# Optimization experiments

Hardware: AMD Instinct MI355X
Metric: run time of the kernel (lower is better)

Reference implementation:

```python
import jax, jax.numpy as jnp
import numpy as np

S_STRIDE = 4
NS = 4
SHIFT_RANGE = 2 * NS + 1  # 9 -> 81 shifts
MASK_THRESH = 10.0


def setup_inputs() -> dict:
    key = jax.random.key(0)
    k1, k2, k3, k4 = jax.random.split(key, 4)
    N, C, H, W = 2, 8, 1024, 1024
    ms_img = jax.random.uniform(k1, (N, C, H, W), dtype=jnp.float32)
    target = jax.random.uniform(k2, (N, C, H, W), dtype=jnp.float32)
    ms_img_o = jax.random.uniform(k3, (N, C, H, W), dtype=jnp.float32)
    fr_pan = jax.random.uniform(k4, (N, 1, H, W), dtype=jnp.float32)
    return {"ms_img": ms_img, "target": target, "ms_img_o": ms_img_o, "fr_pan": fr_pan}


def _min_shift_loss(ms_img, target):
    # Equivalent to torch: reflect-pad target, unfold 9x9 dilated-by-4 windows,
    # per-shift sum_C |ms - shifted_target|, then min over the 81 shifts.
    # Computed with a running min to avoid the (N,C,81,H,W) intermediate.
    N, C, H, W = target.shape
    p = NS * S_STRIDE
    tpad = jnp.pad(target, ((0, 0), (0, 0), (p, p), (p, p)), mode="reflect")
    min_sloss = None
    for i in range(SHIFT_RANGE):
        for j in range(SHIFT_RANGE):
            shifted = tpad[:, :, i * S_STRIDE:i * S_STRIDE + H, j * S_STRIDE:j * S_STRIDE + W]
            sl = jnp.sum(jnp.abs(ms_img - shifted), axis=1)  # (N, H, W)
            min_sloss = sl if min_sloss is None else jnp.minimum(min_sloss, sl)
    return min_sloss


def _normalize(x):
    # min-max normalize to [0,1] over the whole tensor (normalize_torch)
    lo = jnp.min(x)
    hi = jnp.max(x)
    return (x - lo) / (hi - lo)


def reference(ms_img, target, ms_img_o, fr_pan):
    min_sloss = _min_shift_loss(ms_img, target)           # (N, H, W)
    ms_o_gray = jnp.mean(ms_img_o, axis=1)                # (N, H, W)
    mask_gray = _normalize(jnp.abs(ms_o_gray - fr_pan[:, 0])) * 255.0
    mask = mask_gray > MASK_THRESH
    masked_sum = jnp.sum(jnp.where(mask, min_sloss, 0.0))
    cnt = jnp.sum(mask).astype(min_sloss.dtype)
    # mean over masked pixels; 0 if mask empty (matches torch early-return 0)
    return jnp.where(cnt > 0, masked_sum / jnp.maximum(cnt, 1.0), 0.0)
```

## Files before the change

### kernel.cpp

```cpp
#include <hip/hip_runtime.h>

#define WW 1024
#define HH 1024
#define NIMG 2
#define NCH 8
#define HWSZ (HH * WW)
#define CHW (NCH * HWSZ)
#define NBLK_MASK 2048
#define NBLK_MAIN 1024
#define WS_SUM 4096
#define WS_CNT 4097
#define WS_TKT 4098
#define WS_DV16 4352
#define WS_QT (4352 + HWSZ)
#define RECU4 320
#define SLOTU 1280

typedef unsigned int uint;

__device__ __forceinline__ uint pknorm(float a, float b) {
    uint d;
    asm("v_cvt_pknorm_u16_f32 %0, %1, %2" : "=v"(d) : "v"(a), "v"(b));
    return d;
}
__device__ __forceinline__ uint sadu8(uint a, uint b, uint c) {
    uint d;
    asm("v_sad_u8 %0, %1, %2, %3" : "=v"(d) : "v"(a), "v"(b), "v"(c));
    return d;
}
__device__ __forceinline__ uint q8(float x) {
    return (uint)__float2int_rn(x * 255.f);
}
__device__ __forceinline__ int reflect_idx(int t) {
    if (t < 0) t = -t;
    if (t > HH - 1) t = 2 * (HH - 1) - t;
    return t;
}
__device__ __forceinline__ int gp2slot(int gp) {
    return (gp & 1) ? (68 + (gp >> 1)) : (gp >> 1);
}

#define GLD16(g, l)                                                         \
    __builtin_amdgcn_global_load_lds(                                       \
        (const __attribute__((address_space(1))) uint*)(g),                 \
        (__attribute__((address_space(3))) uint*)(l), 16, 0, 0)

__global__ __launch_bounds__(256) void k_quant(const float* __restrict__ tgt,
                                               uint4* __restrict__ qt4) {
    int b = blockIdx.x;
    int t = threadIdx.x;
    int row = b & 1023;
    int np = b >> 10;
    int n = np >> 1, p = np & 1;
    const float* c0 = tgt + (size_t)(n * NCH + 4 * p) * HWSZ + (size_t)row * WW;

    float4 v0 = *(const float4*)(c0 + 4 * t);
    float4 v1 = *(const float4*)(c0 + HWSZ + 4 * t);
    float4 v2 = *(const float4*)(c0 + 2 * HWSZ + 4 * t);
    float4 v3 = *(const float4*)(c0 + 3 * HWSZ + 4 * t);
    uint4 u;
    u.x = q8(v0.x) | (q8(v1.x) << 8) | (q8(v2.x) << 16) | (q8(v3.x) << 24);
    u.y = q8(v0.y) | (q8(v1.y) << 8) | (q8(v2.y) << 16) | (q8(v3.y) << 24);
    u.z = q8(v0.z) | (q8(v1.z) << 8) | (q8(v2.z) << 16) | (q8(v3.z) << 24);
    u.w = q8(v0.w) | (q8(v1.w) << 8) | (q8(v2.w) << 16) | (q8(v3.w) << 24);

    size_t rb = ((size_t)((n << 10) + row)) * 2;
    int h1 = t >> 7;
    int gp = (t & 127) + 4;
    qt4[(rb + h1) * RECU4 + p * 136 + gp2slot(gp)] = u;
    if (t >= 124 && t < 128)
        qt4[(rb + 1) * RECU4 + p * 136 + gp2slot(t - 124)] = u;
    if (t >= 128 && t < 132)
        qt4[(rb + 0) * RECU4 + p * 136 + gp2slot(t - 128 + 132)] = u;
    if (t < 32) {
        int which = t >> 4, m = t & 15;
        int pc = which ? (528 + m) : m;
        int j = which ? (1022 - m) : (16 - m);
        uint val = q8(c0[j]) | (q8(c0[j + HWSZ]) << 8) |
                   (q8(c0[j + 2 * HWSZ]) << 16) | (q8(c0[j + 3 * HWSZ]) << 24);
        uint* recU = (uint*)(qt4 + (rb + which) * RECU4);
        recU[p * 544 + gp2slot(pc >> 2) * 4 + (pc & 3)] = val;
    }
}

__global__ __launch_bounds__(256) void k_mask(const float* __restrict__ msO,
                                              const float* __restrict__ pan,
                                              float* __restrict__ wsF,
                                              uint* __restrict__ dv16) {
    int b = blockIdx.x;
    int gid = b * 256 + threadIdx.x;
    int base = gid * 4;
    int n = base >> 20;
    int hw = base & (HWSZ - 1);
    const float* po = msO + (size_t)n * CHW + hw;
    float sx = 0.f, sy = 0.f, sz = 0.f, sw = 0.f;
#pragma unroll
    for (int c = 0; c < NCH; ++c) {
        float4 v = *(const float4*)(po + c * HWSZ);
        sx += v.x; sy += v.y; sz += v.z; sw += v.w;
    }
    float4 pv = *(const float4*)(pan + (size_t)n * HWSZ + hw);
    float4 d;
    d.x = fabsf(sx * 0.125f - pv.x);
    d.y = fabsf(sy * 0.125f - pv.y);
    d.z = fabsf(sz * 0.125f - pv.z);
    d.w = fabsf(sw * 0.125f - pv.w);
    uint2 dpk;
    dpk.x = pknorm(d.x, d.y);
    dpk.y = pknorm(d.z, d.w);
    *(uint2*)(dv16 + (base >> 1)) = dpk;

    float m = fminf(fminf(d.x, d.y), fminf(d.z, d.w));
    float M = fmaxf(fmaxf(d.x, d.y), fmaxf(d.z, d.w));
#pragma unroll
    for (int off = 32; off > 0; off >>= 1) {
        m = fminf(m, __shfl_down(m, off));
        M = fmaxf(M, __shfl_down(M, off));
    }
    __shared__ float sm[4], sM[4];
    int wid = threadIdx.x >> 6, lane = threadIdx.x & 63;
    if (lane == 0) { sm[wid] = m; sM[wid] = M; }
    __syncthreads();
    if (threadIdx.x == 0) {
        wsF[b] = fminf(fminf(sm[0], sm[1]), fminf(sm[2], sm[3]));
        wsF[2048 + b] = fmaxf(fmaxf(sM[0], sM[1]), fmaxf(sM[2], sM[3]));
        if (b == 0) {
            wsF[WS_SUM] = 0.f;
            wsF[WS_CNT] = 0.f;
            ((unsigned*)wsF)[WS_TKT] = 0u;
        }
    }
}

__global__ __launch_bounds__(64) void k_main(const float* __restrict__ ms,
                                             const uint4* __restrict__ qt4,
                                             float* __restrict__ wsF,
                                             const uint* __restrict__ dv16,
                                             float* __restrict__ out) {
    __shared__ __align__(16) uint ldsU[10 * SLOTU];
    const int t = threadIdx.x;
    const int b = blockIdx.x;
    const int xcd = b & 7;
    const int q = b >> 3;
    const int n = q >> 6;
    const int r = q & 63;
    const int hb = r >> 5;
    const int w = r & 31;
    const int h0 = xcd * 128 + 16 * (w >> 2) + (w & 3);
    const int w0 = hb * 512 + 8 * t;

    float lmin = 1.0e38f, lmax = -1.0e38f;
#pragma unroll
    for (int k = 0; k < 8; ++k) {
        float4 v = ((const float4*)wsF)[k * 64 + t];
        float4 x = ((const float4*)(wsF + 2048))[k * 64 + t];
        lmin = fminf(lmin, fminf(fminf(v.x, v.y), fminf(v.z, v.w)));
        lmax = fmaxf(lmax, fmaxf(fmaxf(x.x, x.y), fmaxf(x.z, x.w)));
    }

    const size_t recStride2 = 2;
    const size_t nBase = ((size_t)n << 10);
#pragma unroll 1
    for (int s = 0; s < 10; ++s) {
        int row = reflect_idx(h0 + 4 * (s - 4));
        const uint* rec = (const uint*)(qt4 + ((nBase + row) * recStride2 + hb) * RECU4);
#pragma unroll
        for (int c = 0; c < 5; ++c)
            GLD16(rec + c * 256 + 4 * t, &ldsU[s * SLOTU + c * 256]);
    }

#pragma unroll
    for (int off = 32; off > 0; off >>= 1) {
        lmin = fminf(lmin, __shfl_xor(lmin, off));
        lmax = fmaxf(lmax, __shfl_xor(lmax, off));
    }
    const float thresh = lmin + (lmax - lmin) * (10.0f / 255.0f);
    const float inv16 = 1.0f / 65535.0f;
    const float inv8 = 1.0f / 255.0f;

    asm volatile("s_waitcnt vmcnt(0)" ::: "memory");

    float lsum = 0.f, lcnt = 0.f;

#pragma unroll 1
    for (int k = 0; k < 4; ++k) {
        const int oh = h0 + 4 * k;

        const float* msBase = ms + (size_t)n * CHW + (size_t)oh * WW + w0;
        float4 A[2][4][2];
#pragma unroll
        for (int p = 0; p < 2; ++p)
#pragma unroll
            for (int cc = 0; cc < 4; ++cc) {
                A[p][cc][0] = *(const float4*)(msBase + (size_t)(4 * p + cc) * HWSZ);
                A[p][cc][1] = *(const float4*)(msBase + (size_t)(4 * p + cc) * HWSZ + 4);
            }
        uint4 dq = *(const uint4*)(dv16 + (((size_t)n * HWSZ + (size_t)oh * WW + w0) >> 1));

        if (k == 1 || k == 2) {
            int prow = reflect_idx(h0 + 4 * (k + 5));
            const uint* rec = (const uint*)(qt4 + ((nBase + prow) * recStride2 + hb) * RECU4);
#pragma unroll
            for (int c = 0; c < 5; ++c)
                GLD16(rec + c * 256 + 4 * t, &ldsU[(k - 1) * SLOTU + c * 256]);
        }

        uint msq[2][8];
#pragma unroll
        for (int p = 0; p < 2; ++p) {
#pragma unroll
            for (int half = 0; half < 2; ++half) {
                float4 c0 = A[p][0][half], c1 = A[p][1][half],
                       c2 = A[p][2][half], c3 = A[p][3][half];
                msq[p][4 * half + 0] = q8(c0.x) | (q8(c1.x) << 8) | (q8(c2.x) << 16) | (q8(c3.x) << 24);
                msq[p][4 * half + 1] = q8(c0.y) | (q8(c1.y) << 8) | (q8(c2.y) << 16) | (q8(c3.y) << 24);
                msq[p][4 * half + 2] = q8(c0.z) | (q8(c1.z) << 8) | (q8(c2.z) << 16) | (q8(c3.z) << 24);
                msq[p][4 * half + 3] = q8(c0.w) | (q8(c1.w) << 8) | (q8(c2.w) << 16) | (q8(c3.w) << 24);
            }
        }

        uint minv[8];
#pragma unroll
        for (int p = 0; p < 8; ++p) minv[p] = 0xffffffffu;

#pragma unroll 1
        for (int di = 0; di < 9; ++di) {
            int slot = k + di; if (slot >= 10) slot -= 10;
            const uint* sb = &ldsU[slot * SLOTU];
            uint4 winE[2][5], winO[2][5];
#pragma unroll
            for (int p = 0; p < 2; ++p)
#pragma unroll
                for (int qq = 0; qq < 5; ++qq) {
                    winE[p][qq] = *(const uint4*)(sb + p * 544 + 4 * (t + qq));
                    winO[p][qq] = *(const uint4*)(sb + p * 544 + 272 + 4 * (t + qq));
                }
            uint acc[8];
#pragma unroll
            for (int dj = 0; dj < 9; ++dj) {
#pragma unroll
                for (int p = 0; p < 8; ++p) acc[p] = 0;
#pragma unroll
                for (int p = 0; p < 2; ++p) {
                    uint4 lo = (dj & 1) ? winO[p][(dj - 1) >> 1] : winE[p][dj >> 1];
                    uint4 hi = (dj & 1) ? winE[p][(dj + 1) >> 1] : winO[p][dj >> 1];
                    acc[0] = sadu8(msq[p][0], lo.x, acc[0]);
                    acc[1] = sadu8(msq[p][1], lo.y, acc[1]);
                    acc[2] = sadu8(msq[p][2], lo.z, acc[2]);
                    acc[3] = sadu8(msq[p][3], lo.w, acc[3]);
                    acc[4] = sadu8(msq[p][4], hi.x, acc[4]);
                    acc[5] = sadu8(msq[p][5], hi.y, acc[5]);
                    acc[6] = sadu8(msq[p][6], hi.z, acc[6]);
                    acc[7] = sadu8(msq[p][7], hi.w, acc[7]);
                }
#pragma unroll
                for (int p = 0; p < 8; ++p) minv[p] = min(minv[p], acc[p]);
            }
        }
        asm volatile("s_waitcnt vmcnt(0)" ::: "memory");

        uint dw[4] = {dq.x, dq.y, dq.z, dq.w};
#pragma unroll
        for (int p = 0; p < 4; ++p) {
            float d0 = (float)(dw[p] & 0xffffu) * inv16;
            float d1 = (float)(dw[p] >> 16) * inv16;
            if (d0 > thresh) { lsum += (float)minv[2 * p] * inv8; lcnt += 1.f; }
            if (d1 > thresh) { lsum += (float)minv[2 * p + 1] * inv8; lcnt += 1.f; }
        }
    }

#pragma unroll
    for (int off = 32; off > 0; off >>= 1) {
        lsum += __shfl_down(lsum, off);
        lcnt += __shfl_down(lcnt, off);
    }
    if (t == 0) {
        atomicAdd(&wsF[WS_SUM], lsum);
        atomicAdd(&wsF[WS_CNT], lcnt);
        __threadfence();
        unsigned tk = atomicAdd((unsigned*)&wsF[WS_TKT], 1u);
        if (tk == NBLK_MAIN - 1) {
            float s = atomicAdd(&wsF[WS_SUM], 0.f);
            float c = atomicAdd(&wsF[WS_CNT], 0.f);
            out[0] = (c > 0.f) ? (s / fmaxf(c, 1.f)) : 0.f;
        }
    }
}

extern "C" void kernel_launch(void* const* d_in, const int* in_sizes, int n_in,
                              void* d_out, int out_size, void* d_ws, size_t ws_size,
                              hipStream_t stream) {
    const float* ms  = (const float*)d_in[0];
    const float* tgt = (const float*)d_in[1];
    const float* msO = (const float*)d_in[2];
    const float* pan = (const float*)d_in[3];
    float* out = (float*)d_out;
    float* wsF = (float*)d_ws;
    uint* dv16 = (uint*)d_ws + WS_DV16;
    uint4* qt4 = (uint4*)((uint*)d_ws + WS_QT);

    k_quant<<<NIMG * 2 * 1024, 256, 0, stream>>>(tgt, qt4);
    k_mask<<<NBLK_MASK, 256, 0, stream>>>(msO, pan, wsF, dv16);
    k_main<<<NBLK_MAIN, 64, 0, stream>>>(ms, qt4, wsF, dv16, out);
}
```

Measured before the change: 273.5 us.

## Stream shifted target rows through double-buffered LDS with two output rows per block

The main kernel now launches twice as many blocks, each computing two output rows instead of four. It streams the ten needed target rows through a two-slot LDS ring, prefetching the next row while computing the current one, and each loaded row feeds both output rows' running minima. This cuts LDS use per block (raising occupancy) and overlaps global loads with SAD compute. In exchange, each block loads ten target rows to serve only two output rows, so total target traffic per output row rises.

```diff
diff --git a/kernel.cpp b/kernel.cpp
--- a/kernel.cpp
+++ b/kernel.cpp
@@ -7,7 +7,7 @@
 #define HWSZ (HH * WW)
 #define CHW (NCH * HWSZ)
 #define NBLK_MASK 2048
-#define NBLK_MAIN 1024
+#define NBLK_MAIN 2048
 #define WS_SUM 4096
 #define WS_CNT 4097
 #define WS_TKT 4098
@@ -137,16 +137,16 @@
                                              float* __restrict__ wsF,
                                              const uint* __restrict__ dv16,
                                              float* __restrict__ out) {
-    __shared__ __align__(16) uint ldsU[10 * SLOTU];
+    __shared__ __align__(16) uint ldsU[2 * SLOTU];
     const int t = threadIdx.x;
     const int b = blockIdx.x;
     const int xcd = b & 7;
     const int q = b >> 3;
-    const int n = q >> 6;
-    const int r = q & 63;
-    const int hb = r >> 5;
-    const int w = r & 31;
-    const int h0 = xcd * 128 + 16 * (w >> 2) + (w & 3);
+    const int n = q >> 7;
+    const int r = q & 127;
+    const int hb = r >> 6;
+    const int w = r & 63;
+    const int h0 = xcd * 128 + 8 * (w >> 2) + (w & 3);
     const int w0 = hb * 512 + 8 * t;
 
     float lmin = 1.0e38f, lmax = -1.0e38f;
@@ -158,16 +158,47 @@
         lmax = fmaxf(lmax, fmaxf(fmaxf(x.x, x.y), fmaxf(x.z, x.w)));
     }
 
-    const size_t recStride2 = 2;
     const size_t nBase = ((size_t)n << 10);
-#pragma unroll 1
-    for (int s = 0; s < 10; ++s) {
-        int row = reflect_idx(h0 + 4 * (s - 4));
-        const uint* rec = (const uint*)(qt4 + ((nBase + row) * recStride2 + hb) * RECU4);
-#pragma unroll
-        for (int c = 0; c < 5; ++c)
-            GLD16(rec + c * 256 + 4 * t, &ldsU[s * SLOTU + c * 256]);
-    }
+#define STAGE(s, slot)                                                      \
+    do {                                                                    \
+        int row_ = reflect_idx(h0 + 4 * ((s) - 4));                         \
+        const uint* rec_ = (const uint*)(qt4 + ((nBase + row_) * 2 + hb) * RECU4); \
+        _Pragma("unroll")                                                   \
+        for (int c_ = 0; c_ < 5; ++c_)                                      \
+            GLD16(rec_ + c_ * 256 + 4 * t, &ldsU[(slot) * SLOTU + c_ * 256]); \
+    } while (0)
+
+    STAGE(0, 0);
+
+    uint msq[2][2][8];
+#pragma unroll
+    for (int k = 0; k < 2; ++k) {
+        const float* msBase = ms + (size_t)n * CHW + (size_t)(h0 + 4 * k) * WW + w0;
+#pragma unroll
+        for (int p = 0; p < 2; ++p) {
+            float4 c0a = *(const float4*)(msBase + (size_t)(4 * p + 0) * HWSZ);
+            float4 c0b = *(const float4*)(msBase + (size_t)(4 * p + 0) * HWSZ + 4);
+            float4 c1a = *(const float4*)(msBase + (size_t)(4 * p + 1) * HWSZ);
+            float4 c1b = *(const float4*)(msBase + (size_t)(4 * p + 1) * HWSZ + 4);
+            float4 c2a = *(const float4*)(msBase + (size_t)(4 * p + 2) * HWSZ);
+            float4 c2b = *(const float4*)(msBase + (size_t)(4 * p + 2) * HWSZ + 4);
+            float4 c3a = *(const float4*)(msBase + (size_t)(4 * p + 3) * HWSZ);
+            float4 c3b = *(const float4*)(msBase + (size_t)(4 * p + 3) * HWSZ + 4);
+            msq[k][p][0] = q8(c0a.x) | (q8(c1a.x) << 8) | (q8(c2a.x) << 16) | (q8(c3a.x) << 24);
+            msq[k][p][1] = q8(c0a.y) | (q8(c1a.y) << 8) | (q8(c2a.y) << 16) | (q8(c3a.y) << 24);
+            msq[k][p][2] = q8(c0a.z) | (q8(c1a.z) << 8) | (q8(c2a.z) << 16) | (q8(c3a.z) << 24);
+            msq[k][p][3] = q8(c0a.w) | (q8(c1a.w) << 8) | (q8(c2a.w) << 16) | (q8(c3a.w) << 24);
+            msq[k][p][4] = q8(c0b.x) | (q8(c1b.x) << 8) | (q8(c2b.x) << 16) | (q8(c3b.x) << 24);
+            msq[k][p][5] = q8(c0b.y) | (q8(c1b.y) << 8) | (q8(c2b.y) << 16) | (q8(c3b.y) << 24);
+            msq[k][p][6] = q8(c0b.z) | (q8(c1b.z) << 8) | (q8(c2b.z) << 16) | (q8(c3b.z) << 24);
+            msq[k][p][7] = q8(c0b.w) | (q8(c1b.w) << 8) | (q8(c2b.w) << 16) | (q8(c3b.w) << 24);
+        }
+    }
+    uint4 dq[2];
+#pragma unroll
+    for (int k = 0; k < 2; ++k)
+        dq[k] = *(const uint4*)(dv16 +
+            (((size_t)n * HWSZ + (size_t)(h0 + 4 * k) * WW + w0) >> 1));
 
 #pragma unroll
     for (int off = 32; off > 0; off >>= 1) {
@@ -175,66 +206,33 @@
         lmax = fmaxf(lmax, __shfl_xor(lmax, off));
     }
     const float thresh = lmin + (lmax - lmin) * (10.0f / 255.0f);
-    const float inv16 = 1.0f / 65535.0f;
-    const float inv8 = 1.0f / 255.0f;
-
-    asm volatile("s_waitcnt vmcnt(0)" ::: "memory");
-
-    float lsum = 0.f, lcnt = 0.f;
+
+    uint minv[2][8];
+#pragma unroll
+    for (int k = 0; k < 2; ++k)
+#pragma unroll
+        for (int p = 0; p < 8; ++p) minv[k][p] = 0xffffffffu;
 
 #pragma unroll 1
-    for (int k = 0; k < 4; ++k) {
-        const int oh = h0 + 4 * k;
-
-        const float* msBase = ms + (size_t)n * CHW + (size_t)oh * WW + w0;
-        float4 A[2][4][2];
+    for (int s = 0; s < 10; ++s) {
+        if (s < 9) {
+            STAGE(s + 1, (s + 1) & 1);
+            asm volatile("s_waitcnt vmcnt(5)" ::: "memory");
+        } else {
+            asm volatile("s_waitcnt vmcnt(0)" ::: "memory");
+        }
+        const uint* sb = &ldsU[(s & 1) * SLOTU];
+        uint4 winE[2][5], winO[2][5];
 #pragma unroll
         for (int p = 0; p < 2; ++p)
 #pragma unroll
-            for (int cc = 0; cc < 4; ++cc) {
-                A[p][cc][0] = *(const float4*)(msBase + (size_t)(4 * p + cc) * HWSZ);
-                A[p][cc][1] = *(const float4*)(msBase + (size_t)(4 * p + cc) * HWSZ + 4);
+            for (int qq = 0; qq < 5; ++qq) {
+                winE[p][qq] = *(const uint4*)(sb + p * 544 + 4 * (t + qq));
+                winO[p][qq] = *(const uint4*)(sb + p * 544 + 272 + 4 * (t + qq));
             }
-        uint4 dq = *(const uint4*)(dv16 + (((size_t)n * HWSZ + (size_t)oh * WW + w0) >> 1));
-
-        if (k == 1 || k == 2) {
-            int prow = reflect_idx(h0 + 4 * (k + 5));
-            const uint* rec = (const uint*)(qt4 + ((nBase + prow) * recStride2 + hb) * RECU4);
-#pragma unroll
-            for (int c = 0; c < 5; ++c)
-                GLD16(rec + c * 256 + 4 * t, &ldsU[(k - 1) * SLOTU + c * 256]);
-        }
-
-        uint msq[2][8];
-#pragma unroll
-        for (int p = 0; p < 2; ++p) {
-#pragma unroll
-            for (int half = 0; half < 2; ++half) {
-                float4 c0 = A[p][0][half], c1 = A[p][1][half],
-                       c2 = A[p][2][half], c3 = A[p][3][half];
-                msq[p][4 * half + 0] = q8(c0.x) | (q8(c1.x) << 8) | (q8(c2.x) << 16) | (q8(c3.x) << 24);
-                msq[p][4 * half + 1] = q8(c0.y) | (q8(c1.y) << 8) | (q8(c2.y) << 16) | (q8(c3.y) << 24);
-                msq[p][4 * half + 2] = q8(c0.z) | (q8(c1.z) << 8) | (q8(c2.z) << 16) | (q8(c3.z) << 24);
-                msq[p][4 * half + 3] = q8(c0.w) | (q8(c1.w) << 8) | (q8(c2.w) << 16) | (q8(c3.w) << 24);
-            }
-        }
-
-        uint minv[8];
-#pragma unroll
-        for (int p = 0; p < 8; ++p) minv[p] = 0xffffffffu;
-
-#pragma unroll 1
-        for (int di = 0; di < 9; ++di) {
-            int slot = k + di; if (slot >= 10) slot -= 10;
-            const uint* sb = &ldsU[slot * SLOTU];
-            uint4 winE[2][5], winO[2][5];
-#pragma unroll
-            for (int p = 0; p < 2; ++p)
-#pragma unroll
-                for (int qq = 0; qq < 5; ++qq) {
-                    winE[p][qq] = *(const uint4*)(sb + p * 544 + 4 * (t + qq));
-                    winO[p][qq] = *(const uint4*)(sb + p * 544 + 272 + 4 * (t + qq));
-                }
+#pragma unroll
+        for (int k = 0; k < 2; ++k) {
+            if (s < k || s - k > 8) continue;
             uint acc[8];
 #pragma unroll
             for (int dj = 0; dj < 9; ++dj) {
@@ -244,31 +242,35 @@
                 for (int p = 0; p < 2; ++p) {
                     uint4 lo = (dj & 1) ? winO[p][(dj - 1) >> 1] : winE[p][dj >> 1];
                     uint4 hi = (dj & 1) ? winE[p][(dj + 1) >> 1] : winO[p][dj >> 1];
-                    acc[0] = sadu8(msq[p][0], lo.x, acc[0]);
-                    acc[1] = sadu8(msq[p][1], lo.y, acc[1]);
-                    acc[2] = sadu8(msq[p][2], lo.z, acc[2]);
-                    acc[3] = sadu8(msq[p][3], lo.w, acc[3]);
-                    acc[4] = sadu8(msq[p][4], hi.x, acc[4]);
-                    acc[5] = sadu8(msq[p][5], hi.y, acc[5]);
-                    acc[6] = sadu8(msq[p][6], hi.z, acc[6]);
-                    acc[7] = sadu8(msq[p][7], hi.w, acc[7]);
+                    acc[0] = sadu8(msq[k][p][0], lo.x, acc[0]);
+                    acc[1] = sadu8(msq[k][p][1], lo.y, acc[1]);
+                    acc[2] = sadu8(msq[k][p][2], lo.z, acc[2]);
+                    acc[3] = sadu8(msq[k][p][3], lo.w, acc[3]);
+                    acc[4] = sadu8(msq[k][p][4], hi.x, acc[4]);
+                    acc[5] = sadu8(msq[k][p][5], hi.y, acc[5]);
+                    acc[6] = sadu8(msq[k][p][6], hi.z, acc[6]);
+                    acc[7] = sadu8(msq[k][p][7], hi.w, acc[7]);
                 }
 #pragma unroll
-                for (int p = 0; p < 8; ++p) minv[p] = min(minv[p], acc[p]);
+                for (int p = 0; p < 8; ++p) minv[k][p] = min(minv[k][p], acc[p]);
             }
         }
-        asm volatile("s_waitcnt vmcnt(0)" ::: "memory");
-
-        uint dw[4] = {dq.x, dq.y, dq.z, dq.w};
+    }
+
+    const float inv16 = 1.0f / 65535.0f;
+    const float inv8 = 1.0f / 255.0f;
+    float lsum = 0.f, lcnt = 0.f;
+#pragma unroll
+    for (int k = 0; k < 2; ++k) {
+        uint dw[4] = {dq[k].x, dq[k].y, dq[k].z, dq[k].w};
 #pragma unroll
         for (int p = 0; p < 4; ++p) {
             float d0 = (float)(dw[p] & 0xffffu) * inv16;
             float d1 = (float)(dw[p] >> 16) * inv16;
-            if (d0 > thresh) { lsum += (float)minv[2 * p] * inv8; lcnt += 1.f; }
-            if (d1 > thresh) { lsum += (float)minv[2 * p + 1] * inv8; lcnt += 1.f; }
-        }
-    }
-
+            if (d0 > thresh) { lsum += (float)minv[k][2 * p] * inv8; lcnt += 1.f; }
+            if (d1 > thresh) { lsum += (float)minv[k][2 * p + 1] * inv8; lcnt += 1.f; }
+        }
+    }
 #pragma unroll
     for (int off = 32; off > 0; off >>= 1) {
         lsum += __shfl_down(lsum, off);
@@ -285,6 +287,7 @@
             out[0] = (c > 0.f) ? (s / fmaxf(c, 1.f)) : 0.f;
         }
     }
+#undef STAGE
 }
 
 extern "C" void kernel_launch(void* const* d_in, const int* in_sizes, int n_in,
```

Result: slower. 292.4 us (+6.9%).
